# Kernel tuning notes

Measured on AMD Instinct MI355X. Metric: run time of the kernel, lower is better.

Reference implementation:

```python
import jax, jax.numpy as jnp
import numpy as np

NUM_USERS = 100000
NUM_ITEMS = 50000
N_NODES = NUM_USERS + NUM_ITEMS
NUM_COMMUNITY = 64
N_LAYERS = 3
NNZ = 2400000
BATCH = 8192
NEG_SLOPE = 0.1
EPS = 1e-12


def setup_inputs() -> dict:
    key = jax.random.key(0)
    ks = jax.random.split(key, 9)
    stdv = 1.0 / np.sqrt(NUM_COMMUNITY)
    return {
        "users": jax.random.randint(ks[0], (BATCH,), 0, NUM_USERS, dtype=jnp.int64 if jax.config.jax_enable_x64 else jnp.int32).astype(jnp.int32),
        "adjacent_items": jax.random.randint(ks[1], (BATCH,), 0, NUM_ITEMS).astype(jnp.int32),
        "weak_items": jax.random.randint(ks[2], (BATCH,), 0, NUM_ITEMS).astype(jnp.int32),
        "strong_items": jax.random.randint(ks[3], (BATCH,), 0, NUM_ITEMS).astype(jnp.int32),
        "edge_rows": jax.random.randint(ks[4], (NNZ,), 0, N_NODES).astype(jnp.int32),
        "edge_cols": jax.random.randint(ks[5], (NNZ,), 0, N_NODES).astype(jnp.int32),
        "edge_vals": jax.random.uniform(ks[6], (NNZ,), dtype=jnp.float32),
        "user_preference": jax.random.uniform(ks[7], (NUM_USERS, NUM_COMMUNITY), dtype=jnp.float32, minval=-stdv, maxval=stdv),
        "item_preference": jax.random.uniform(ks[8], (NUM_ITEMS, NUM_COMMUNITY), dtype=jnp.float32, minval=-stdv, maxval=stdv),
    }


def _lrelu_l2norm(x):
    # leaky_relu(neg_slope=0.1) then L2-normalize along last dim (torch F.normalize semantics)
    x = jnp.where(x >= 0, x, NEG_SLOPE * x)
    norm = jnp.sqrt(jnp.sum(x * x, axis=-1, keepdims=True))
    return x / jnp.maximum(norm, EPS)


def reference(users, adjacent_items, weak_items, strong_items,
              edge_rows, edge_cols, edge_vals,
              user_preference, item_preference):
    # ---- computer(): LightGCN-style propagation over sparse adjacency ----
    pref = _lrelu_l2norm(jnp.concatenate([user_preference, item_preference], axis=0))  # [N, C]
    acc = pref
    p = pref
    for _ in range(N_LAYERS):
        # sparse.mm(Graph, p): gather source rows, scale by edge values, scatter-add into dest rows
        msg = edge_vals[:, None] * p[edge_cols]                      # [nnz, C]
        p = jax.ops.segment_sum(msg, edge_rows, num_segments=N_NODES)  # [N, C]
        p = _lrelu_l2norm(p)
        acc = acc + p
    merged = acc / (N_LAYERS + 1)  # mean over stacked layers
    users_pref = merged[:NUM_USERS]
    items_pref = merged[NUM_USERS:]

    # ---- forward(): per-pair dot products + sigmoid ----
    u = users_pref[users]  # [B, C]

    def score(items):
        return jax.nn.sigmoid(jnp.sum(u * items_pref[items], axis=-1))

    # stack of (adjacent, weak, strong) gamma preferences, shape [3, B]
    return jnp.stack([score(adjacent_items), score(weak_items), score(strong_items)], axis=0)
```

## Files before the change

### kernel.cpp

```cpp
#include <hip/hip_runtime.h>
#include <hip/hip_fp16.h>
#include <math.h>

#define D 64
#define NUM_USERS 100000
#define NUM_ITEMS 50000
#define N_NODES 150000
#define NNZ 2400000
#define BATCH 8192
#define NEG_SLOPE 0.1f
#define EPS_NRM 1e-12f

#define NB2     293
#define RPB     512
#define NCHUNK  256
#define CH      9376
#define NHT     (NB2 * NCHUNK)
#define NBH     (NHT / 256)
#define CAP     10240
#define VSCALE  16383.f

typedef unsigned short ushort_t;
typedef int   iv4 __attribute__((ext_vector_type(4)));
typedef float fv4 __attribute__((ext_vector_type(4)));

__device__ __forceinline__ float wave_sum64(float v) {
    #pragma unroll
    for (int off = 32; off > 0; off >>= 1)
        v += __shfl_xor(v, off, 64);
    return v;
}

__device__ __forceinline__ int wave_sum64_i(int v) {
    #pragma unroll
    for (int off = 32; off > 0; off >>= 1)
        v += __shfl_xor(v, off, 64);
    return v;
}

__device__ __forceinline__ float h2f_lo(unsigned u) {
    return __half2float(__ushort_as_half((unsigned short)(u & 0xFFFFu)));
}
__device__ __forceinline__ float h2f_hi(unsigned u) {
    return __half2float(__ushort_as_half((unsigned short)(u >> 16)));
}


__global__ void __launch_bounds__(512) bucket_hist(const int* __restrict__ rows,
                                                   int* __restrict__ ht) {
    __shared__ int hist[NB2];
    int c = blockIdx.x, tid = threadIdx.x;
    for (int b = tid; b < NB2; b += 512) hist[b] = 0;
    __syncthreads();
    int base = c * CH;
    int n = NNZ - base; if (n > CH) n = CH;
    const iv4* r4 = (const iv4*)(rows + base);
    for (int i = tid; i < (n >> 2); i += 512) {
        iv4 r = __builtin_nontemporal_load(&r4[i]);
        atomicAdd(&hist[r.x >> 9], 1);
        atomicAdd(&hist[r.y >> 9], 1);
        atomicAdd(&hist[r.z >> 9], 1);
        atomicAdd(&hist[r.w >> 9], 1);
    }
    __syncthreads();
    for (int b = tid; b < NB2; b += 512) ht[b * NCHUNK + c] = hist[b];
}

__global__ void scan1_kernel(const int* __restrict__ in, int* __restrict__ out,
                             int* __restrict__ bsums, int n) {
    int tid = threadIdx.x, gid = blockIdx.x * 256 + tid;
    int v = (gid < n) ? in[gid] : 0;
    int lane = tid & 63, w = tid >> 6;
    int s = v;
    #pragma unroll
    for (int off = 1; off < 64; off <<= 1) {
        int t = __shfl_up(s, off, 64);
        if (lane >= off) s += t;
    }
    __shared__ int wsum[4];
    if (lane == 63) wsum[w] = s;
    __syncthreads();
    if (tid == 0) {
        int a = 0;
        #pragma unroll
        for (int i = 0; i < 4; i++) { int t = wsum[i]; wsum[i] = a; a += t; }
    }
    __syncthreads();
    int incl = s + wsum[w];
    if (gid < n) out[gid] = incl - v;
    if (tid == 255) bsums[blockIdx.x] = incl;
}

__global__ void scan3_kernel(int* __restrict__ out, const int* __restrict__ bsums, int n) {
    __shared__ int wtot[4];
    __shared__ int total;
    int b = blockIdx.x, tid = threadIdx.x;
    int lane = tid & 63, w = tid >> 6;
    int partial = 0;
    for (int i = tid; i < b; i += 256) partial += bsums[i];
    partial = wave_sum64_i(partial);
    if (lane == 0) wtot[w] = partial;
    __syncthreads();
    if (tid == 0) total = wtot[0] + wtot[1] + wtot[2] + wtot[3];
    __syncthreads();
    int gid = b * 256 + tid;
    if (gid < n) out[gid] += total;
}

__global__ void __launch_bounds__(1024) bucket_scatter(
        const int* __restrict__ rows, const int* __restrict__ cols,
        const float* __restrict__ vals, const int* __restrict__ hoff,
        uint2* __restrict__ es8) {
    __shared__ int cur[NB2];
    int c = blockIdx.x, tid = threadIdx.x;
    if (tid < NB2) cur[tid] = hoff[tid * NCHUNK + c];
    __syncthreads();
    int base = c * CH;
    int n = NNZ - base; if (n > CH) n = CH;
    const iv4* r4 = (const iv4*)(rows + base);
    const iv4* c4 = (const iv4*)(cols + base);
    const fv4* v4 = (const fv4*)(vals + base);
    for (int i = tid; i < (n >> 2); i += 1024) {
        iv4 r  = __builtin_nontemporal_load(&r4[i]);
        iv4 cc = __builtin_nontemporal_load(&c4[i]);
        fv4 v  = __builtin_nontemporal_load(&v4[i]);
        int p;
        p = atomicAdd(&cur[r.x >> 9], 1);
        es8[p] = make_uint2((unsigned)cc.x | ((unsigned)(v.x * VSCALE + 0.5f) << 18),
                            (unsigned)(r.x & (RPB - 1)));
        p = atomicAdd(&cur[r.y >> 9], 1);
        es8[p] = make_uint2((unsigned)cc.y | ((unsigned)(v.y * VSCALE + 0.5f) << 18),
                            (unsigned)(r.y & (RPB - 1)));
        p = atomicAdd(&cur[r.z >> 9], 1);
        es8[p] = make_uint2((unsigned)cc.z | ((unsigned)(v.z * VSCALE + 0.5f) << 18),
                            (unsigned)(r.z & (RPB - 1)));
        p = atomicAdd(&cur[r.w >> 9], 1);
        es8[p] = make_uint2((unsigned)cc.w | ((unsigned)(v.w * VSCALE + 0.5f) << 18),
                            (unsigned)(r.w & (RPB - 1)));
    }
}

__global__ void __launch_bounds__(1024) bucket_sort(const uint2* __restrict__ es8,
                                                    const int* __restrict__ hoff,
                                                    unsigned* __restrict__ es,
                                                    int* __restrict__ rowptr) {
    __shared__ int      hist[RPB];
    __shared__ int      wsum[8];
    __shared__ unsigned outbuf[CAP];
    int b = blockIdx.x, tid = threadIdx.x;
    int beg = hoff[b * NCHUNK];
    int end = (b == NB2 - 1) ? NNZ : hoff[(b + 1) * NCHUNK];
    if (tid < RPB) hist[tid] = 0;
    __syncthreads();
    for (int i = beg + tid; i < end; i += 1024)
        atomicAdd(&hist[es8[i].y], 1);
    __syncthreads();
    int excl = 0;
    if (tid < RPB) {
        int v = hist[tid];
        int lane = tid & 63, w = tid >> 6;
        int s = v;
        #pragma unroll
        for (int off = 1; off < 64; off <<= 1) {
            int t = __shfl_up(s, off, 64);
            if (lane >= off) s += t;
        }
        if (lane == 63) wsum[w] = s;
        excl = s - v;
    }
    __syncthreads();
    if (tid == 0) {
        int a = 0;
        #pragma unroll
        for (int i = 0; i < 8; i++) { int t = wsum[i]; wsum[i] = a; a += t; }
    }
    __syncthreads();
    if (tid < RPB) {
        excl += wsum[tid >> 6];
        int r = b * RPB + tid;
        if (r <= N_NODES) rowptr[r] = beg + excl;
        hist[tid] = excl;
    }
    __syncthreads();
    for (int i = beg + tid; i < end; i += 1024) {
        uint2 kv = es8[i];
        int d = atomicAdd(&hist[kv.y], 1);
        outbuf[d] = kv.x;
    }
    __syncthreads();
    int n = end - beg;
    for (int i = tid; i < n; i += 1024)
        es[beg + i] = outbuf[i];
}

__global__ void init_kernel(const float* __restrict__ upref,
                            const float* __restrict__ ipref,
                            __half* __restrict__ p0) {
    int row  = blockIdx.x * 4 + (threadIdx.x >> 6);
    int lane = threadIdx.x & 63;
    if (row >= N_NODES) return;
    float x = (row < NUM_USERS) ? upref[(size_t)row * D + lane]
                                : ipref[(size_t)(row - NUM_USERS) * D + lane];
    x = (x >= 0.f) ? x : NEG_SLOPE * x;
    float norm = sqrtf(wave_sum64(x * x));
    float y = x / fmaxf(norm, EPS_NRM);
    p0[(size_t)row * D + lane] = __float2half(y);
}

__device__ __forceinline__ void acc8(float a[8], float v, uint4 q) {
    a[0] = fmaf(v, h2f_lo(q.x), a[0]);
    a[1] = fmaf(v, h2f_hi(q.x), a[1]);
    a[2] = fmaf(v, h2f_lo(q.y), a[2]);
    a[3] = fmaf(v, h2f_hi(q.y), a[3]);
    a[4] = fmaf(v, h2f_lo(q.z), a[4]);
    a[5] = fmaf(v, h2f_hi(q.z), a[5]);
    a[6] = fmaf(v, h2f_lo(q.w), a[6]);
    a[7] = fmaf(v, h2f_hi(q.w), a[7]);
}

__global__ void gather_kernel(const int* __restrict__ rowptr,
                              const unsigned* __restrict__ es,
                              const __half* __restrict__ p,
                              __half* __restrict__ pn) {
    int tid  = threadIdx.x;
    int row  = blockIdx.x * 8 + (tid >> 5);
    if (row >= N_NODES) return;
    int hl   = tid & 31;
    int sub  = hl >> 3;
    int fl   = hl & 7;
    int beg = rowptr[row], end = rowptr[row + 1];

    float a[8];
    #pragma unroll
    for (int k = 0; k < 8; k++) a[k] = 0.f;

    const float vs = 1.f / VSCALE;
    int e = beg + sub;
    while (e + 4 < end) {
        unsigned ev0 = es[e];
        unsigned ev1 = es[e + 4];
        const uint4 q0 = *(const uint4*)(p + (((ev0 & 0x3FFFFu) << 6) | (fl << 3)));
        const uint4 q1 = *(const uint4*)(p + (((ev1 & 0x3FFFFu) << 6) | (fl << 3)));
        float v0 = (float)(ev0 >> 18) * vs;
        float v1 = (float)(ev1 >> 18) * vs;
        acc8(a, v0, q0);
        acc8(a, v1, q1);
        e += 8;
    }
    if (e < end) {
        unsigned ev = es[e];
        const uint4 q = *(const uint4*)(p + (((ev & 0x3FFFFu) << 6) | (fl << 3)));
        float v = (float)(ev >> 18) * vs;
        acc8(a, v, q);
    }

    bool s0 = (sub & 1) != 0, s1 = (sub & 2) != 0;
    float b1[4];
    #pragma unroll
    for (int j = 0; j < 4; j++) {
        int c4 = (j >> 1) * 4, bb = j & 1;
        float keep = s0 ? a[c4 + 2 + bb] : a[c4 + bb];
        float send = s0 ? a[c4 + bb]     : a[c4 + 2 + bb];
        b1[j] = keep + __shfl_xor(send, 8, 64);
    }
    float cf[2];
    #pragma unroll
    for (int bb = 0; bb < 2; bb++) {
        float keep = s1 ? b1[2 + bb] : b1[bb];
        float send = s1 ? b1[bb]     : b1[2 + bb];
        cf[bb] = keep + __shfl_xor(send, 16, 64);
    }
    float y0 = (cf[0] >= 0.f) ? cf[0] : NEG_SLOPE * cf[0];
    float y1 = (cf[1] >= 0.f) ? cf[1] : NEG_SLOPE * cf[1];
    float ss = fmaf(y0, y0, y1 * y1);
    ss += __shfl_xor(ss, 16, 64);
    ss += __shfl_xor(ss, 8, 64);
    ss += __shfl_xor(ss, 4, 64);
    ss += __shfl_xor(ss, 2, 64);
    ss += __shfl_xor(ss, 1, 64);
    float inv = 1.f / fmaxf(sqrtf(ss), EPS_NRM);
    __half2 o = __floats2half2_rn(y0 * inv, y1 * inv);
    *(__half2*)(pn + (size_t)row * D + fl * 8 + 2 * sub) = o;
}

__global__ void score_kernel(const int* __restrict__ users,
                             const int* __restrict__ it0,
                             const int* __restrict__ it1,
                             const int* __restrict__ it2,
                             const __half* __restrict__ p0,
                             const __half* __restrict__ p1,
                             const __half* __restrict__ p2,
                             const __half* __restrict__ p3,
                             float* __restrict__ out) {
    int b    = blockIdx.x * 4 + (threadIdx.x >> 6);
    int lane = threadIdx.x & 63;
    if (b >= BATCH) return;
    int u = users[b];
    size_t uo = (size_t)u * D + lane;
    float uf = __half2float(p0[uo]) + __half2float(p1[uo])
             + __half2float(p2[uo]) + __half2float(p3[uo]);

    int its[3];
    its[0] = it0[b]; its[1] = it1[b]; its[2] = it2[b];
    #pragma unroll
    for (int k = 0; k < 3; k++) {
        size_t io = (size_t)(NUM_USERS + its[k]) * D + lane;
        float itf = __half2float(p0[io]) + __half2float(p1[io])
                  + __half2float(p2[io]) + __half2float(p3[io]);
        float s = wave_sum64(uf * itf) * 0.0625f;
        if (lane == 0)
            out[k * BATCH + b] = 1.f / (1.f + expf(-s));
    }
}

extern "C" void kernel_launch(void* const* d_in, const int* in_sizes, int n_in,
                              void* d_out, int out_size, void* d_ws, size_t ws_size,
                              hipStream_t stream) {
    const int*   users  = (const int*)  d_in[0];
    const int*   adj    = (const int*)  d_in[1];
    const int*   weak   = (const int*)  d_in[2];
    const int*   strong = (const int*)  d_in[3];
    const int*   erows  = (const int*)  d_in[4];
    const int*   ecols  = (const int*)  d_in[5];
    const float* evals  = (const float*)d_in[6];
    const float* upref  = (const float*)d_in[7];
    const float* ipref  = (const float*)d_in[8];
    float* out = (float*)d_out;

    const size_t rowElems = (size_t)N_NODES * D;

    char* base = (char*)d_ws;
    size_t off = 0;
    auto alloc = [&](size_t bytes) {
        char* p = base + off;
        off = (off + bytes + 255) & ~(size_t)255;
        return (void*)p;
    };
    __half*   p0     = (__half*)  alloc(rowElems * sizeof(__half));
    __half*   p1     = (__half*)  alloc(rowElems * sizeof(__half));
    __half*   p2     = (__half*)  alloc(rowElems * sizeof(__half));
    __half*   p3     = (__half*)  alloc(rowElems * sizeof(__half));
    unsigned* es     = (unsigned*)alloc((size_t)NNZ * sizeof(unsigned));
    int*      ht     = (int*)     alloc((size_t)NHT * sizeof(int));
    int*      hoff   = (int*)     alloc((size_t)NHT * sizeof(int));
    int*      rowptr = (int*)     alloc((N_NODES + 2) * sizeof(int));
    int*      bsums  = (int*)     alloc(1024 * sizeof(int));
    uint2*    es8t   = (uint2*)p2;

    bucket_hist   <<<NCHUNK, 512, 0, stream>>>(erows, ht);
    scan1_kernel  <<<NBH, 256, 0, stream>>>(ht, hoff, bsums, NHT);
    scan3_kernel  <<<NBH, 256, 0, stream>>>(hoff, bsums, NHT);
    bucket_scatter<<<NCHUNK, 1024, 0, stream>>>(erows, ecols, evals, hoff, es8t);
    bucket_sort   <<<NB2, 1024, 0, stream>>>(es8t, hoff, es, rowptr);

    init_kernel<<<(N_NODES + 3) / 4, 256, 0, stream>>>(upref, ipref, p0);
    gather_kernel<<<N_NODES / 8, 256, 0, stream>>>(rowptr, es, p0, p1);
    gather_kernel<<<N_NODES / 8, 256, 0, stream>>>(rowptr, es, p1, p2);
    gather_kernel<<<N_NODES / 8, 256, 0, stream>>>(rowptr, es, p2, p3);

    score_kernel<<<(BATCH + 3) / 4, 256, 0, stream>>>(users, adj, weak, strong,
                                                      p0, p1, p2, p3, out);
}
```

Baseline: 318.9 us.

## Replace global histogram scan with fixed-capacity buckets and fuse init into scatter

Drops the separate histogram, two-pass scan and init kernels. Each chunk counts its bucket entries in shared memory, then reserves space with a global atomic into a fixed-capacity slot per bucket (CAPB). The normalization init runs as extra blocks of the same launch, and rowptr becomes begin/end int2 pairs because buckets are no longer contiguous. This removes several launches and their global traffic, but reads rows twice within the block, relies on no bucket exceeding CAPB entries (true for uniform random inputs), and makes edge order within a bucket nondeterministic.

```diff
diff --git a/kernel.cpp b/kernel.cpp
--- a/kernel.cpp
+++ b/kernel.cpp
@@ -15,8 +15,7 @@
 #define RPB     512
 #define NCHUNK  256
 #define CH      9376
-#define NHT     (NB2 * NCHUNK)
-#define NBH     (NHT / 256)
+#define CAPB    9472
 #define CAP     10240
 #define VSCALE  16383.f
 
@@ -31,13 +30,6 @@
     return v;
 }
 
-__device__ __forceinline__ int wave_sum64_i(int v) {
-    #pragma unroll
-    for (int off = 32; off > 0; off >>= 1)
-        v += __shfl_xor(v, off, 64);
-    return v;
-}
-
 __device__ __forceinline__ float h2f_lo(unsigned u) {
     return __half2float(__ushort_as_half((unsigned short)(u & 0xFFFFu)));
 }
@@ -45,83 +37,52 @@
     return __half2float(__ushort_as_half((unsigned short)(u >> 16)));
 }
 
-
-__global__ void __launch_bounds__(512) bucket_hist(const int* __restrict__ rows,
-                                                   int* __restrict__ ht) {
-    __shared__ int hist[NB2];
-    int c = blockIdx.x, tid = threadIdx.x;
-    for (int b = tid; b < NB2; b += 512) hist[b] = 0;
-    __syncthreads();
-    int base = c * CH;
+__global__ void __launch_bounds__(1024) scatter_init(
+        const int* __restrict__ rows, const int* __restrict__ cols,
+        const float* __restrict__ vals, int* __restrict__ gcur,
+        uint2* __restrict__ es8,
+        const float* __restrict__ upref, const float* __restrict__ ipref,
+        __half* __restrict__ p0) {
+    __shared__ int cnt[NB2];
+    __shared__ int cur[NB2];
+    int blk = blockIdx.x, tid = threadIdx.x;
+
+    if (blk >= NCHUNK) {
+        int row  = (blk - NCHUNK) * 16 + (tid >> 6);
+        int lane = tid & 63;
+        if (row >= N_NODES) return;
+        float x = (row < NUM_USERS) ? upref[(size_t)row * D + lane]
+                                    : ipref[(size_t)(row - NUM_USERS) * D + lane];
+        x = (x >= 0.f) ? x : NEG_SLOPE * x;
+        float norm = sqrtf(wave_sum64(x * x));
+        float y = x / fmaxf(norm, EPS_NRM);
+        p0[(size_t)row * D + lane] = __float2half(y);
+        return;
+    }
+
+    for (int b = tid; b < NB2; b += 1024) cnt[b] = 0;
+    __syncthreads();
+    int base = blk * CH;
     int n = NNZ - base; if (n > CH) n = CH;
     const iv4* r4 = (const iv4*)(rows + base);
-    for (int i = tid; i < (n >> 2); i += 512) {
-        iv4 r = __builtin_nontemporal_load(&r4[i]);
-        atomicAdd(&hist[r.x >> 9], 1);
-        atomicAdd(&hist[r.y >> 9], 1);
-        atomicAdd(&hist[r.z >> 9], 1);
-        atomicAdd(&hist[r.w >> 9], 1);
-    }
-    __syncthreads();
-    for (int b = tid; b < NB2; b += 512) ht[b * NCHUNK + c] = hist[b];
-}
-
-__global__ void scan1_kernel(const int* __restrict__ in, int* __restrict__ out,
-                             int* __restrict__ bsums, int n) {
-    int tid = threadIdx.x, gid = blockIdx.x * 256 + tid;
-    int v = (gid < n) ? in[gid] : 0;
-    int lane = tid & 63, w = tid >> 6;
-    int s = v;
-    #pragma unroll
-    for (int off = 1; off < 64; off <<= 1) {
-        int t = __shfl_up(s, off, 64);
-        if (lane >= off) s += t;
-    }
-    __shared__ int wsum[4];
-    if (lane == 63) wsum[w] = s;
-    __syncthreads();
-    if (tid == 0) {
-        int a = 0;
-        #pragma unroll
-        for (int i = 0; i < 4; i++) { int t = wsum[i]; wsum[i] = a; a += t; }
-    }
-    __syncthreads();
-    int incl = s + wsum[w];
-    if (gid < n) out[gid] = incl - v;
-    if (tid == 255) bsums[blockIdx.x] = incl;
-}
-
-__global__ void scan3_kernel(int* __restrict__ out, const int* __restrict__ bsums, int n) {
-    __shared__ int wtot[4];
-    __shared__ int total;
-    int b = blockIdx.x, tid = threadIdx.x;
-    int lane = tid & 63, w = tid >> 6;
-    int partial = 0;
-    for (int i = tid; i < b; i += 256) partial += bsums[i];
-    partial = wave_sum64_i(partial);
-    if (lane == 0) wtot[w] = partial;
-    __syncthreads();
-    if (tid == 0) total = wtot[0] + wtot[1] + wtot[2] + wtot[3];
-    __syncthreads();
-    int gid = b * 256 + tid;
-    if (gid < n) out[gid] += total;
-}
-
-__global__ void __launch_bounds__(1024) bucket_scatter(
-        const int* __restrict__ rows, const int* __restrict__ cols,
-        const float* __restrict__ vals, const int* __restrict__ hoff,
-        uint2* __restrict__ es8) {
-    __shared__ int cur[NB2];
-    int c = blockIdx.x, tid = threadIdx.x;
-    if (tid < NB2) cur[tid] = hoff[tid * NCHUNK + c];
-    __syncthreads();
-    int base = c * CH;
-    int n = NNZ - base; if (n > CH) n = CH;
-    const iv4* r4 = (const iv4*)(rows + base);
+    for (int i = tid; i < (n >> 2); i += 1024) {
+        iv4 r = r4[i];
+        atomicAdd(&cnt[r.x >> 9], 1);
+        atomicAdd(&cnt[r.y >> 9], 1);
+        atomicAdd(&cnt[r.z >> 9], 1);
+        atomicAdd(&cnt[r.w >> 9], 1);
+    }
+    __syncthreads();
+    if (tid < NB2) {
+        int c = cnt[tid];
+        int off = (c > 0) ? atomicAdd(&gcur[tid], c) : 0;
+        cur[tid] = tid * CAPB + off;
+    }
+    __syncthreads();
     const iv4* c4 = (const iv4*)(cols + base);
     const fv4* v4 = (const fv4*)(vals + base);
     for (int i = tid; i < (n >> 2); i += 1024) {
-        iv4 r  = __builtin_nontemporal_load(&r4[i]);
+        iv4 r  = r4[i];
         iv4 cc = __builtin_nontemporal_load(&c4[i]);
         fv4 v  = __builtin_nontemporal_load(&v4[i]);
         int p;
@@ -141,23 +102,24 @@
 }
 
 __global__ void __launch_bounds__(1024) bucket_sort(const uint2* __restrict__ es8,
-                                                    const int* __restrict__ hoff,
+                                                    const int* __restrict__ gcur,
                                                     unsigned* __restrict__ es,
-                                                    int* __restrict__ rowptr) {
+                                                    int2* __restrict__ rowptr2) {
     __shared__ int      hist[RPB];
     __shared__ int      wsum[8];
     __shared__ unsigned outbuf[CAP];
     int b = blockIdx.x, tid = threadIdx.x;
-    int beg = hoff[b * NCHUNK];
-    int end = (b == NB2 - 1) ? NNZ : hoff[(b + 1) * NCHUNK];
+    int base = b * CAPB;
+    int fill = gcur[b];
+    int end  = base + fill;
     if (tid < RPB) hist[tid] = 0;
     __syncthreads();
-    for (int i = beg + tid; i < end; i += 1024)
+    for (int i = base + tid; i < end; i += 1024)
         atomicAdd(&hist[es8[i].y], 1);
     __syncthreads();
-    int excl = 0;
+    int excl = 0, v = 0;
     if (tid < RPB) {
-        int v = hist[tid];
+        v = hist[tid];
         int lane = tid & 63, w = tid >> 6;
         int s = v;
         #pragma unroll
@@ -178,33 +140,19 @@
     if (tid < RPB) {
         excl += wsum[tid >> 6];
         int r = b * RPB + tid;
-        if (r <= N_NODES) rowptr[r] = beg + excl;
+        if (r < N_NODES)
+            rowptr2[r] = make_int2(base + excl, base + excl + v);
         hist[tid] = excl;
     }
     __syncthreads();
-    for (int i = beg + tid; i < end; i += 1024) {
+    for (int i = base + tid; i < end; i += 1024) {
         uint2 kv = es8[i];
         int d = atomicAdd(&hist[kv.y], 1);
         outbuf[d] = kv.x;
     }
     __syncthreads();
-    int n = end - beg;
-    for (int i = tid; i < n; i += 1024)
-        es[beg + i] = outbuf[i];
-}
-
-__global__ void init_kernel(const float* __restrict__ upref,
-                            const float* __restrict__ ipref,
-                            __half* __restrict__ p0) {
-    int row  = blockIdx.x * 4 + (threadIdx.x >> 6);
-    int lane = threadIdx.x & 63;
-    if (row >= N_NODES) return;
-    float x = (row < NUM_USERS) ? upref[(size_t)row * D + lane]
-                                : ipref[(size_t)(row - NUM_USERS) * D + lane];
-    x = (x >= 0.f) ? x : NEG_SLOPE * x;
-    float norm = sqrtf(wave_sum64(x * x));
-    float y = x / fmaxf(norm, EPS_NRM);
-    p0[(size_t)row * D + lane] = __float2half(y);
+    for (int i = tid; i < fill; i += 1024)
+        es[base + i] = outbuf[i];
 }
 
 __device__ __forceinline__ void acc8(float a[8], float v, uint4 q) {
@@ -218,7 +166,7 @@
     a[7] = fmaf(v, h2f_hi(q.w), a[7]);
 }
 
-__global__ void gather_kernel(const int* __restrict__ rowptr,
+__global__ void gather_kernel(const int2* __restrict__ rowptr2,
                               const unsigned* __restrict__ es,
                               const __half* __restrict__ p,
                               __half* __restrict__ pn) {
@@ -228,7 +176,8 @@
     int hl   = tid & 31;
     int sub  = hl >> 3;
     int fl   = hl & 7;
-    int beg = rowptr[row], end = rowptr[row + 1];
+    int2 rp  = rowptr2[row];
+    int beg = rp.x, end = rp.y;
 
     float a[8];
     #pragma unroll
@@ -336,27 +285,23 @@
         off = (off + bytes + 255) & ~(size_t)255;
         return (void*)p;
     };
-    __half*   p0     = (__half*)  alloc(rowElems * sizeof(__half));
-    __half*   p1     = (__half*)  alloc(rowElems * sizeof(__half));
-    __half*   p2     = (__half*)  alloc(rowElems * sizeof(__half));
-    __half*   p3     = (__half*)  alloc(rowElems * sizeof(__half));
-    unsigned* es     = (unsigned*)alloc((size_t)NNZ * sizeof(unsigned));
-    int*      ht     = (int*)     alloc((size_t)NHT * sizeof(int));
-    int*      hoff   = (int*)     alloc((size_t)NHT * sizeof(int));
-    int*      rowptr = (int*)     alloc((N_NODES + 2) * sizeof(int));
-    int*      bsums  = (int*)     alloc(1024 * sizeof(int));
-    uint2*    es8t   = (uint2*)p2;
-
-    bucket_hist   <<<NCHUNK, 512, 0, stream>>>(erows, ht);
-    scan1_kernel  <<<NBH, 256, 0, stream>>>(ht, hoff, bsums, NHT);
-    scan3_kernel  <<<NBH, 256, 0, stream>>>(hoff, bsums, NHT);
-    bucket_scatter<<<NCHUNK, 1024, 0, stream>>>(erows, ecols, evals, hoff, es8t);
-    bucket_sort   <<<NB2, 1024, 0, stream>>>(es8t, hoff, es, rowptr);
-
-    init_kernel<<<(N_NODES + 3) / 4, 256, 0, stream>>>(upref, ipref, p0);
-    gather_kernel<<<N_NODES / 8, 256, 0, stream>>>(rowptr, es, p0, p1);
-    gather_kernel<<<N_NODES / 8, 256, 0, stream>>>(rowptr, es, p1, p2);
-    gather_kernel<<<N_NODES / 8, 256, 0, stream>>>(rowptr, es, p2, p3);
+    __half*   p0      = (__half*)  alloc(rowElems * sizeof(__half));
+    __half*   p1      = (__half*)  alloc(rowElems * sizeof(__half));
+    __half*   p2      = (__half*)  alloc(rowElems * sizeof(__half));
+    __half*   p3      = (__half*)  alloc(rowElems * sizeof(__half));
+    unsigned* es      = (unsigned*)alloc((size_t)NB2 * CAPB * 4);
+    int2*     rowptr2 = (int2*)    alloc((size_t)N_NODES * sizeof(int2));
+    int*      gcur    = (int*)     alloc(NB2 * sizeof(int));
+    uint2*    es8t    = (uint2*)p2;
+
+    hipMemsetAsync(gcur, 0, NB2 * sizeof(int), stream);
+    scatter_init<<<NCHUNK + (N_NODES + 15) / 16, 1024, 0, stream>>>(
+        erows, ecols, evals, gcur, es8t, upref, ipref, p0);
+    bucket_sort<<<NB2, 1024, 0, stream>>>(es8t, gcur, es, rowptr2);
+
+    gather_kernel<<<N_NODES / 8, 256, 0, stream>>>(rowptr2, es, p0, p1);
+    gather_kernel<<<N_NODES / 8, 256, 0, stream>>>(rowptr2, es, p1, p2);
+    gather_kernel<<<N_NODES / 8, 256, 0, stream>>>(rowptr2, es, p2, p3);
 
     score_kernel<<<(BATCH + 3) / 4, 256, 0, stream>>>(users, adj, weak, strong,
                                                       p0, p1, p2, p3, out);
```

New measurement: 321.0 us. Within noise of the previous version (+0.7%).
